# Kernel optimization log

Measured on AMD Instinct MI355X. Metric: run time of the kernel, lower is better.

## Reference

```python
import jax, jax.numpy as jnp
import numpy as np

B, T, R, C = 16, 128, 8192, 91   # batch, num_targets, num_reg (proposals), num_classes
RED = 16                          # feature-map stride ('reduction')
IOU_THRESH = 0.7


def setup_inputs() -> dict:
    key = jax.random.key(0)
    ks = jax.random.split(key, 7)
    # Ground-truth boxes [top, left, bottom, right] with strictly positive h/w.
    u = jax.random.uniform(ks[0], (B, T, 4))
    top = u[..., 0] * 400.0
    left = u[..., 1] * 400.0
    h = 32.0 + u[..., 2] * 200.0
    w = 32.0 + u[..., 3] * 200.0
    bboxes = jnp.stack([top, left, top + h, left + w], axis=-1)
    # NMS proposals = jittered copies of random GT boxes, so a realistic fraction has IoU > 0.7.
    tidx = jax.random.randint(ks[1], (B, R), 0, T)
    base = jnp.take_along_axis(bboxes, tidx[:, :, None], axis=1)
    nms_reg = base + jax.random.normal(ks[2], (B, R, 4)) * 4.0
    rcnn_reg = jax.random.normal(ks[3], (B, R, 4)) * 0.1
    rcnn_cls = jax.random.normal(ks[4], (B, R, C))
    nms_cls = jax.random.normal(ks[5], (B, R, 2))  # unused by the loss, kept for API fidelity
    classes = jax.random.randint(ks[6], (B, T), 0, C).astype(jnp.int32)
    return {"nms_reg": nms_reg, "nms_cls": nms_cls, "rcnn_reg": rcnn_reg,
            "rcnn_cls": rcnn_cls, "bboxes": bboxes, "classes": classes, "reduction": RED}


def _iou(a, b):
    # a: [B,1,R,4] proposals, b: [B,T,1,4] targets; box = [top,left,bottom,right]
    it = jnp.maximum(a[..., 0], b[..., 0])
    il = jnp.maximum(a[..., 1], b[..., 1])
    ib = jnp.minimum(a[..., 2], b[..., 2])
    ir = jnp.minimum(a[..., 3], b[..., 3])
    inter = jnp.clip(ib - it, 0.0) * jnp.clip(ir - il, 0.0)
    area_a = (a[..., 2] - a[..., 0]) * (a[..., 3] - a[..., 1])
    area_b = (b[..., 2] - b[..., 0]) * (b[..., 3] - b[..., 1])
    return inter / (area_a + area_b - inter)


def _smooth_l1(x):
    ax = jnp.abs(x)
    return jnp.where(ax < 1.0, 0.5 * x * x, ax - 0.5)


def _masked_mean(v, mask, count):
    return jnp.sum(v * mask) / jnp.maximum(count, 1.0)


def reference(nms_reg, nms_cls, rcnn_reg, rcnn_cls, bboxes, classes, reduction):
    # Pairwise IoU [B, T, R]; original materialized O(B*T*R*4) and O(B*T*R*C) expands.
    iou = _iou(nms_reg[:, None, :, :], bboxes[:, :, None, :])
    # Original sorts along the target dim and takes the last slice == max/argmax.
    max_iou = jnp.max(iou, axis=1)                # [B, R]
    idx = jnp.argmax(iou, axis=1)                 # [B, R] best target per proposal
    max_bboxes = jnp.take_along_axis(bboxes, idx[:, :, None], axis=1)  # [B, R, 4]
    max_classes = jnp.take_along_axis(classes, idx, axis=1)            # [B, R]
    # gather of rcnn_reg / rcnn_cls along the target dim is an identity (they don't depend on it)
    mask = (max_iou > IOU_THRESH).astype(rcnn_reg.dtype)
    count = jnp.sum(mask)

    # CrossEntropyLoss (mean over positives)
    logp = jax.nn.log_softmax(rcnn_cls, axis=-1)
    nll = -jnp.take_along_axis(logp, max_classes[..., None], axis=-1)[..., 0]
    cls_loss = _masked_mean(nll, mask, count)

    # Categorical accuracy over positives
    correct = (jnp.argmax(rcnn_cls, axis=-1) == max_classes).astype(rcnn_reg.dtype)
    accuracy = _masked_mean(correct, mask, count)

    # SmoothL1 on normalized offsets vs rcnn_reg (== masked_reg in original)
    red = jnp.asarray(reduction, rcnn_reg.dtype)
    rounded = jnp.round(max_bboxes / red) * red
    hgt = rounded[..., 2] - rounded[..., 0]
    wid = rounded[..., 3] - rounded[..., 1]
    hgt = jnp.where(hgt == 0.0, 1.0, hgt)  # guard; masked-out rows may have degenerate boxes
    wid = jnp.where(wid == 0.0, 1.0, wid)
    reg_loss = (
        _masked_mean(_smooth_l1(rcnn_reg[..., 0] - (max_bboxes[..., 0] - rounded[..., 0]) / hgt), mask, count)
        + _masked_mean(_smooth_l1(rcnn_reg[..., 1] - (max_bboxes[..., 1] - rounded[..., 1]) / wid), mask, count)
        + _masked_mean(_smooth_l1(rcnn_reg[..., 2] - (max_bboxes[..., 2] - rounded[..., 2]) / hgt), mask, count)
        + _masked_mean(_smooth_l1(rcnn_reg[..., 3] - (max_bboxes[..., 3] - rounded[..., 3]) / wid), mask, count)
    )

    pos = (count > 0.0).astype(rcnn_reg.dtype)  # replaces the .nonzero() branch
    return (cls_loss * pos, reg_loss * pos, accuracy * pos)
```

## Files before the change

### kernel.cpp

```cpp
#include <hip/hip_runtime.h>
#include <hip/hip_bf16.h>

#define NB 16
#define NT 128
#define NR 8192
#define NC 91
#define XTH (0.7f / 1.7f)

#define TILES 8
#define GRID_MAIN (NB * NR / (16 * TILES))
#define BLK_PER_B (GRID_MAIN / NB)

__device__ __forceinline__ float fastdiv(float a, float b) {
    return a * __builtin_amdgcn_rcpf(b);
}
__device__ __forceinline__ float smooth_l1(float x) {
    float ax = fabsf(x);
    return ax < 1.0f ? 0.5f * x * x : ax - 0.5f;
}

#define LOADT(S, it_)                                                          \
    {                                                                          \
        const size_t p_ = pbase + (size_t)(it_) * 16;                          \
        pr##S = ((const float4*)nms_reg)[p_];                                  \
        const float* row_ = rcnn_cls + p_ * NC;                                \
        v##S##0 = row_[l];                                                     \
        v##S##1 = row_[l + 16];                                                \
        v##S##2 = row_[l + 32];                                                \
        v##S##3 = row_[l + 48];                                                \
        v##S##4 = row_[l + 64];                                                \
        v##S##5 = v5ok ? row_[c5] : -INFINITY;                                 \
    }

#define PROC(S, T)                                                             \
    {                                                                          \
        const float area_a = (pr##S.z - pr##S.x) * (pr##S.w - pr##S.y);        \
        unsigned int bu = 0u;                                                  \
        _Pragma("unroll")                                                      \
        for (int j = 0; j < 8; ++j) {                                          \
            const float4 t = tb[j];                                            \
            const float itp = fmaxf(pr##S.x, t.x), il = fmaxf(pr##S.y, t.y);   \
            const float ib  = fminf(pr##S.z, t.z), ir = fminf(pr##S.w, t.w);   \
            const float inter = fmaxf(ib - itp, 0.f) * fmaxf(ir - il, 0.f);    \
            const float x = fastdiv(inter, area_a + areaB[j]);                 \
            bu = max(bu, (__float_as_uint(x) & 0xFFFFFF80u)                    \
                         | (127u - (unsigned int)(l + 16 * j)));               \
        }                                                                      \
        _Pragma("unroll")                                                      \
        for (int mk = 8; mk; mk >>= 1) bu = max(bu, __shfl_xor(bu, mk, 16));   \
        float sv = 1.0f, lc = 0.0f;                                            \
        unsigned int meta = 0u;                                                \
        if (__uint_as_float(bu & 0xFFFFFF80u) > XTH) {                         \
            const int bidx = 127 - (int)(bu & 127u);                           \
            const int cls  = scls[bidx];                                       \
            sv = __expf(v##S##0) + __expf(v##S##1) + __expf(v##S##2)           \
               + __expf(v##S##3) + __expf(v##S##4) + __expf(v##S##5);          \
            float mv = fmaxf(fmaxf(fmaxf(v##S##0, v##S##1),                    \
                                   fmaxf(v##S##2, v##S##3)),                   \
                             fmaxf(v##S##4, v##S##5));                         \
            _Pragma("unroll")                                                  \
            for (int mk = 8; mk; mk >>= 1) {                                   \
                sv += __shfl_xor(sv, mk, 16);                                  \
                mv  = fmaxf(mv, __shfl_xor(mv, mk, 16));                       \
            }                                                                  \
            const int jj = cls >> 4;                                           \
            float val = v##S##0;                                               \
            val = (jj == 1) ? v##S##1 : val;                                   \
            val = (jj == 2) ? v##S##2 : val;                                   \
            val = (jj == 3) ? v##S##3 : val;                                   \
            val = (jj == 4) ? v##S##4 : val;                                   \
            val = (jj == 5) ? v##S##5 : val;                                   \
            lc = __shfl(val, cls & 15, 16);                                    \
            meta = (unsigned int)bidx | 128u | ((lc == mv) ? 256u : 0u);       \
        }                                                                      \
        if (l == 0)                                                            \
            stash[w][((T) << 2) | (grp & 3)] =                                 \
                make_float4(__uint_as_float(meta), sv, lc, 0.f);               \
    }

__global__ __launch_bounds__(256) void frcnn_main(
    const float* __restrict__ nms_reg,
    const float* __restrict__ rcnn_reg,
    const float* __restrict__ rcnn_cls,
    const float* __restrict__ bboxes,
    const int* __restrict__ classes,
    const int* __restrict__ reduction,
    float4* __restrict__ part)
{
    __shared__ float4 sbox[NT];
    __shared__ int    scls[NT];
    __shared__ float4 stash[4][32];
    __shared__ float4 sred[4];

    const int b     = blockIdx.x / BLK_PER_B;
    const int tile0 = (blockIdx.x % BLK_PER_B) * TILES;
    const int grp   = threadIdx.x >> 4;
    const int l     = threadIdx.x & 15;
    const int w     = threadIdx.x >> 6;

    if (threadIdx.x < NT) {
        sbox[threadIdx.x] = ((const float4*)bboxes)[b * NT + threadIdx.x];
        scls[threadIdx.x] = classes[b * NT + threadIdx.x];
    }
    __syncthreads();

    float4 tb[8];
    float  areaB[8];
    #pragma unroll
    for (int j = 0; j < 8; ++j) {
        tb[j]    = sbox[l + 16 * j];
        areaB[j] = (tb[j].z - tb[j].x) * (tb[j].w - tb[j].y);
    }

    const int rv = *reduction;
    float redv;
    if (rv >= 1 && rv <= 65536) redv = (float)rv;
    else redv = __int_as_float(rv);
    const float rredv = __builtin_amdgcn_rcpf(redv);

    const int  c5   = l + 80;
    const bool v5ok = (c5 < NC);

    const size_t pbase = (size_t)b * NR + (size_t)tile0 * 16 + grp;

    float4 prA, prB;
    float vA0, vA1, vA2, vA3, vA4, vA5;
    float vB0, vB1, vB2, vB3, vB4, vB5;

    LOADT(A, 0)
    LOADT(B, 1)
    PROC(A, 0)
    LOADT(A, 2)
    PROC(B, 1)
    LOADT(B, 3)
    PROC(A, 2)
    LOADT(A, 4)
    PROC(B, 3)
    LOADT(B, 5)
    PROC(A, 4)
    LOADT(A, 6)
    PROC(B, 5)
    LOADT(B, 7)
    PROC(A, 6)
    PROC(B, 7)

    float cnt = 0.f, nll = 0.f, reg = 0.f, corr = 0.f;
    const int L = threadIdx.x & 63;
    if (L < 32) {
        const float4 st = stash[w][L];
        const unsigned int meta = __float_as_uint(st.x);
        if (meta & 128u) {
            const int bidx = (int)(meta & 127u);
            cnt  = 1.f;
            corr = (meta & 256u) ? 1.f : 0.f;
            nll  = __logf(st.y) - st.z;

            const float4 bb = sbox[bidx];
            const float rd0 = rintf(bb.x * rredv) * redv;
            const float rd1 = rintf(bb.y * rredv) * redv;
            const float rd2 = rintf(bb.z * rredv) * redv;
            const float rd3 = rintf(bb.w * rredv) * redv;
            float hgt = rd2 - rd0; if (hgt == 0.f) hgt = 1.f;
            float wid = rd3 - rd1; if (wid == 0.f) wid = 1.f;
            const float rh = __builtin_amdgcn_rcpf(hgt);
            const float rw = __builtin_amdgcn_rcpf(wid);

            const int    tl = L >> 2;
            const size_t p  = (size_t)b * NR + (size_t)(tile0 + tl) * 16
                            + (unsigned)(4 * w + (L & 3));
            const float4 rr = ((const float4*)rcnn_reg)[p];
            reg = smooth_l1(rr.x - (bb.x - rd0) * rh)
                + smooth_l1(rr.y - (bb.y - rd1) * rw)
                + smooth_l1(rr.z - (bb.z - rd2) * rh)
                + smooth_l1(rr.w - (bb.w - rd3) * rw);
        }
    }

    #pragma unroll
    for (int mk = 16; mk; mk >>= 1) {
        cnt  += __shfl_xor(cnt,  mk, 32);
        nll  += __shfl_xor(nll,  mk, 32);
        reg  += __shfl_xor(reg,  mk, 32);
        corr += __shfl_xor(corr, mk, 32);
    }
    if (L == 0) sred[w] = make_float4(cnt, nll, reg, corr);
    __syncthreads();
    if (threadIdx.x == 0) {
        float4 t = make_float4(0.f, 0.f, 0.f, 0.f);
        #pragma unroll
        for (int i = 0; i < 4; ++i) {
            t.x += sred[i].x; t.y += sred[i].y; t.z += sred[i].z; t.w += sred[i].w;
        }
        part[blockIdx.x] = t;
    }
}

__global__ __launch_bounds__(1024) void frcnn_reduce(
    const float4* __restrict__ part, float* __restrict__ out)
{
    __shared__ float4 sw[16];
    float4 s = make_float4(0.f, 0.f, 0.f, 0.f);
    for (int i = threadIdx.x; i < GRID_MAIN; i += 1024) {
        const float4 p = part[i];
        s.x += p.x; s.y += p.y; s.z += p.z; s.w += p.w;
    }
    #pragma unroll
    for (int off = 32; off > 0; off >>= 1) {
        s.x += __shfl_down(s.x, off);
        s.y += __shfl_down(s.y, off);
        s.z += __shfl_down(s.z, off);
        s.w += __shfl_down(s.w, off);
    }
    const int lane = threadIdx.x & 63;
    const int w    = threadIdx.x >> 6;
    if (lane == 0) sw[w] = s;
    __syncthreads();
    if (threadIdx.x == 0) {
        float4 t = make_float4(0.f, 0.f, 0.f, 0.f);
        #pragma unroll
        for (int i = 0; i < 16; ++i) {
            t.x += sw[i].x; t.y += sw[i].y; t.z += sw[i].z; t.w += sw[i].w;
        }
        const float pos   = (t.x > 0.f) ? 1.f : 0.f;
        const float denom = fmaxf(t.x, 1.f);
        out[0] = t.y / denom * pos;
        out[1] = t.z / denom * pos;
        out[2] = t.w / denom * pos;
    }
}

extern "C" void kernel_launch(void* const* d_in, const int* in_sizes, int n_in,
                              void* d_out, int out_size, void* d_ws, size_t ws_size,
                              hipStream_t stream) {
    const float* nms_reg  = (const float*)d_in[0];
    const float* rcnn_reg = (const float*)d_in[2];
    const float* rcnn_cls = (const float*)d_in[3];
    const float* bboxes   = (const float*)d_in[4];
    const int*   classes  = (const int*)d_in[5];
    const int*   red      = (const int*)d_in[6];

    float4* part = (float4*)d_ws;

    frcnn_main<<<GRID_MAIN, 256, 0, stream>>>(nms_reg, rcnn_reg, rcnn_cls, bboxes,
                                              classes, red, part);
    frcnn_reduce<<<1, 1024, 0, stream>>>(part, (float*)d_out);
}
```

Measured before the change: 22.92 us.

## Use DPP row rotations for 16-lane reductions and defer label logit gather

Replaces the shfl_xor butterfly reductions over 16-lane groups with DPP row_ror rotations, fused into one chain that reduces the IoU argmax key, the softmax exp-sum and the max logit together. The exp-sum and max are now computed unconditionally for every proposal instead of only for positives. The label logit is no longer picked via a select chain and shuffle; the class index is packed into the stash metadata and the logit is re-read from global memory in the epilogue. This removes LDS-based cross-lane traffic and a branch-dependent second reduction, at the cost of always doing six exps and an extra scattered global load per positive.

```diff
diff --git a/kernel.cpp b/kernel.cpp
--- a/kernel.cpp
+++ b/kernel.cpp
@@ -18,6 +18,14 @@
     float ax = fabsf(x);
     return ax < 1.0f ? 0.5f * x * x : ax - 0.5f;
 }
+
+#define RORU(x, C) ((unsigned int)__builtin_amdgcn_update_dpp(0, (int)(x), (C), 0xF, 0xF, false))
+#define RORF(x, C) __uint_as_float(RORU(__float_as_uint(x), (C)))
+
+#define ROTSTEP(bu, sv, mv, C)                                                 \
+    bu = max(bu, RORU(bu, C));                                                 \
+    sv = sv + RORF(sv, C);                                                     \
+    mv = fmaxf(mv, RORF(mv, C));
 
 #define LOADT(S, it_)                                                          \
     {                                                                          \
@@ -39,43 +47,32 @@
         _Pragma("unroll")                                                      \
         for (int j = 0; j < 8; ++j) {                                          \
             const float4 t = tb[j];                                            \
+            const float S_  = area_a + (t.z - t.x) * (t.w - t.y);              \
             const float itp = fmaxf(pr##S.x, t.x), il = fmaxf(pr##S.y, t.y);   \
             const float ib  = fminf(pr##S.z, t.z), ir = fminf(pr##S.w, t.w);   \
             const float inter = fmaxf(ib - itp, 0.f) * fmaxf(ir - il, 0.f);    \
-            const float x = fastdiv(inter, area_a + areaB[j]);                 \
+            const float x = fastdiv(inter, S_);                                \
             bu = max(bu, (__float_as_uint(x) & 0xFFFFFF80u)                    \
                          | (127u - (unsigned int)(l + 16 * j)));               \
         }                                                                      \
-        _Pragma("unroll")                                                      \
-        for (int mk = 8; mk; mk >>= 1) bu = max(bu, __shfl_xor(bu, mk, 16));   \
-        float sv = 1.0f, lc = 0.0f;                                            \
+        float sv = __expf(v##S##0) + __expf(v##S##1) + __expf(v##S##2)         \
+                 + __expf(v##S##3) + __expf(v##S##4) + __expf(v##S##5);        \
+        float mv = fmaxf(fmaxf(fmaxf(v##S##0, v##S##1),                        \
+                               fmaxf(v##S##2, v##S##3)),                       \
+                         fmaxf(v##S##4, v##S##5));                             \
+        ROTSTEP(bu, sv, mv, 0x128)                                  \
+        ROTSTEP(bu, sv, mv, 0x124)                                  \
+        ROTSTEP(bu, sv, mv, 0x122)                                  \
+        ROTSTEP(bu, sv, mv, 0x121)                                  \
         unsigned int meta = 0u;                                                \
         if (__uint_as_float(bu & 0xFFFFFF80u) > XTH) {                         \
             const int bidx = 127 - (int)(bu & 127u);                           \
             const int cls  = scls[bidx];                                       \
-            sv = __expf(v##S##0) + __expf(v##S##1) + __expf(v##S##2)           \
-               + __expf(v##S##3) + __expf(v##S##4) + __expf(v##S##5);          \
-            float mv = fmaxf(fmaxf(fmaxf(v##S##0, v##S##1),                    \
-                                   fmaxf(v##S##2, v##S##3)),                   \
-                             fmaxf(v##S##4, v##S##5));                         \
-            _Pragma("unroll")                                                  \
-            for (int mk = 8; mk; mk >>= 1) {                                   \
-                sv += __shfl_xor(sv, mk, 16);                                  \
-                mv  = fmaxf(mv, __shfl_xor(mv, mk, 16));                       \
-            }                                                                  \
-            const int jj = cls >> 4;                                           \
-            float val = v##S##0;                                               \
-            val = (jj == 1) ? v##S##1 : val;                                   \
-            val = (jj == 2) ? v##S##2 : val;                                   \
-            val = (jj == 3) ? v##S##3 : val;                                   \
-            val = (jj == 4) ? v##S##4 : val;                                   \
-            val = (jj == 5) ? v##S##5 : val;                                   \
-            lc = __shfl(val, cls & 15, 16);                                    \
-            meta = (unsigned int)bidx | 128u | ((lc == mv) ? 256u : 0u);       \
+            meta = (unsigned int)bidx | 128u | ((unsigned int)cls << 9);       \
         }                                                                      \
         if (l == 0)                                                            \
             stash[w][((T) << 2) | (grp & 3)] =                                 \
-                make_float4(__uint_as_float(meta), sv, lc, 0.f);               \
+                make_float4(__uint_as_float(meta), sv, mv, 0.f);               \
     }
 
 __global__ __launch_bounds__(256) void frcnn_main(
@@ -105,12 +102,8 @@
     __syncthreads();
 
     float4 tb[8];
-    float  areaB[8];
     #pragma unroll
-    for (int j = 0; j < 8; ++j) {
-        tb[j]    = sbox[l + 16 * j];
-        areaB[j] = (tb[j].z - tb[j].x) * (tb[j].w - tb[j].y);
-    }
+    for (int j = 0; j < 8; ++j) tb[j] = sbox[l + 16 * j];
 
     const int rv = *reduction;
     float redv;
@@ -151,9 +144,14 @@
         const unsigned int meta = __float_as_uint(st.x);
         if (meta & 128u) {
             const int bidx = (int)(meta & 127u);
+            const int cls  = (int)((meta >> 9) & 127u);
+            const int tl   = L >> 2;
+            const size_t p = (size_t)b * NR + (size_t)(tile0 + tl) * 16
+                           + (unsigned)(4 * w + (L & 3));
+            const float lc = rcnn_cls[p * NC + cls];
             cnt  = 1.f;
-            corr = (meta & 256u) ? 1.f : 0.f;
-            nll  = __logf(st.y) - st.z;
+            nll  = __logf(st.y) - lc;
+            corr = (lc == st.z) ? 1.f : 0.f;
 
             const float4 bb = sbox[bidx];
             const float rd0 = rintf(bb.x * rredv) * redv;
@@ -165,9 +163,6 @@
             const float rh = __builtin_amdgcn_rcpf(hgt);
             const float rw = __builtin_amdgcn_rcpf(wid);
 
-            const int    tl = L >> 2;
-            const size_t p  = (size_t)b * NR + (size_t)(tile0 + tl) * 16
-                            + (unsigned)(4 * w + (L & 3));
             const float4 rr = ((const float4*)rcnn_reg)[p];
             reg = smooth_l1(rr.x - (bb.x - rd0) * rh)
                 + smooth_l1(rr.y - (bb.y - rd1) * rw)
```

New measurement: 21.98 us. -4.1%, faster.
